# Kernel optimization log

Hardware: AMD Instinct MI355X
Metric: run time of the kernel (lower is better)

## Reference

```python
import jax, jax.numpy as jnp
import numpy as np

N = 100000   # num_rows
M = 50000    # num_cols
D = 32       # embed_dim
E = 5000000  # num observed edges


def setup_inputs() -> dict:
    key = jax.random.key(0)
    ks = jax.random.split(key, 9)
    bound = 1.0 / np.sqrt(D)
    row_embed = jax.random.uniform(ks[0], (N, D), minval=-bound, maxval=bound, dtype=jnp.float32)
    col_embed = jax.random.uniform(ks[1], (M, D), minval=-bound, maxval=bound, dtype=jnp.float32)
    # kaiming_uniform_ with nonlinearity='relu': bound = sqrt(6 / fan_in)
    kb = np.sqrt(6.0 / D)
    W0 = jax.random.uniform(ks[2], (D, D), minval=-kb, maxval=kb, dtype=jnp.float32)
    W1 = jax.random.uniform(ks[3], (D, D), minval=-kb, maxval=kb, dtype=jnp.float32)
    W2 = jax.random.uniform(ks[4], (D, D), minval=-kb, maxval=kb, dtype=jnp.float32)
    b0 = jnp.zeros((D,), jnp.float32)
    b1 = jnp.zeros((D,), jnp.float32)
    b2 = jnp.zeros((D,), jnp.float32)
    edge_index = jax.random.randint(ks[5], (2, E), 0, N + M, dtype=jnp.int64)
    return {"row_embed": row_embed, "col_embed": col_embed,
            "W0": W0, "b0": b0, "W1": W1, "b1": b1, "W2": W2, "b2": b2,
            "edge_index": edge_index}


def reference(row_embed, col_embed, W0, b0, W1, b1, W2, b2, edge_index):
    num_nodes = N + M
    x = jnp.concatenate([row_embed, col_embed], axis=0)  # [N+M, D]
    # add self loops
    loop = jnp.arange(num_nodes, dtype=edge_index.dtype)
    src = jnp.concatenate([edge_index[0], loop])
    dst = jnp.concatenate([edge_index[1], loop])
    for W, b in ((W0, b0), (W1, b1), (W2, b2)):
        h = x @ W.T + b                       # dense linear [N+M, D]
        msg = h[src]                          # gather source features [E+N+M, D]
        agg = jax.ops.segment_sum(msg, dst, num_segments=num_nodes)
        x = jax.nn.relu(agg)
    return (x[:N], x[N:])
```

## Files before the change

### kernel.cpp

```cpp
#include <hip/hip_runtime.h>
#include <hip/hip_fp16.h>

#define N_ROWS 100000
#define NNODES 150000
#define D 32
#define NEDGE 5000000
#define BINSHIFT 7
#define BINSZ 128
#define NBINS 1172
#define NBLK 512
#define SCT 1024
#define CPB ((NEDGE + NBLK - 1) / NBLK)
#define NCOUNTS (NBINS * NBLK)
#define SCAN_ITEMS 1024
#define NSCAN (NCOUNTS / SCAN_ITEMS)

#define NB 8
#define BDIV 18750

#define LIN_T 128
#define LIN_RPB 256
#define LIN_GRID ((NNODES + LIN_RPB - 1) / LIN_RPB)


__global__ void count_kernel(const int* __restrict__ dst, int* __restrict__ counts) {
    __shared__ int h[4 * NBINS];
    const int t = threadIdx.x;
    const int sub = ((t >> 6) & 3) * NBINS;
    for (int b = t; b < 4 * NBINS; b += SCT) h[b] = 0;
    __syncthreads();
    const int e0 = blockIdx.x * CPB;
    const int e1 = min(e0 + CPB, NEDGE);
    for (int i = e0 + t; i < e1; i += SCT) atomicAdd(&h[sub + (dst[i] >> BINSHIFT)], 1);
    __syncthreads();
    for (int b = t; b < NBINS; b += SCT)
        counts[b * NBLK + blockIdx.x] = h[b] + h[NBINS + b] + h[2 * NBINS + b] + h[3 * NBINS + b];
}


__global__ void scanA(const int* __restrict__ counts, int* __restrict__ partials) {
    __shared__ int s[256];
    const int t = threadIdx.x;
    const int base = blockIdx.x * SCAN_ITEMS + t * 4;
    int sum = 0;
#pragma unroll
    for (int k = 0; k < 4; ++k) sum += counts[base + k];
    s[t] = sum;
    __syncthreads();
    for (int off = 128; off > 0; off >>= 1) {
        if (t < off) s[t] += s[t + off];
        __syncthreads();
    }
    if (t == 0) partials[blockIdx.x] = s[0];
}

__global__ void scanB(int* __restrict__ partials) {
    __shared__ int s[256];
    __shared__ int carry;
    const int t = threadIdx.x;
    if (t == 0) carry = 0;
    __syncthreads();
    for (int c = 0; c < (NSCAN + 255) / 256; ++c) {
        int idx = c * 256 + t;
        int v = (idx < NSCAN) ? partials[idx] : 0;
        s[t] = v;
        __syncthreads();
        for (int off = 1; off < 256; off <<= 1) {
            int tmp = (t >= off) ? s[t - off] : 0;
            __syncthreads();
            s[t] += tmp;
            __syncthreads();
        }
        if (idx < NSCAN) partials[idx] = carry + s[t] - v;
        __syncthreads();
        if (t == 0) carry += s[255];
        __syncthreads();
    }
}

__global__ void scanC(const int* __restrict__ counts, const int* __restrict__ partials,
                      int* __restrict__ bases, int* __restrict__ binPtr) {
    __shared__ int s[256];
    const int t = threadIdx.x;
    const int base = blockIdx.x * SCAN_ITEMS + t * 4;
    int c[4];
    int sum = 0;
#pragma unroll
    for (int k = 0; k < 4; ++k) { c[k] = counts[base + k]; sum += c[k]; }
    s[t] = sum;
    __syncthreads();
    for (int off = 1; off < 256; off <<= 1) {
        int v = (t >= off) ? s[t - off] : 0;
        __syncthreads();
        s[t] += v;
        __syncthreads();
    }
    int run = partials[blockIdx.x] + ((t == 0) ? 0 : s[t - 1]);
#pragma unroll
    for (int k = 0; k < 4; ++k) {
        int idx = base + k;
        bases[idx] = run;
        if ((idx & (NBLK - 1)) == 0) binPtr[idx / NBLK] = run;
        run += c[k];
    }
    if (blockIdx.x == 0 && t == 0) binPtr[NBINS] = NEDGE;
}


__global__ void __launch_bounds__(SCT, 2)
scatter3(const int* __restrict__ src, const int* __restrict__ dst,
         const int* __restrict__ bases, unsigned int* __restrict__ binned) {
    __shared__ int cnt[NBINS];
    __shared__ int lb[NBINS + 1];
    __shared__ int gb[NBINS];
    __shared__ int ssum[SCT];
    __shared__ unsigned int staged[CPB];

    const int t = threadIdx.x;
    const int e0 = blockIdx.x * CPB;
    const int e1 = min(e0 + CPB, NEDGE);
    const int n = e1 - e0;

    for (int b = t; b < NBINS; b += SCT) {
        cnt[b] = 0;
        gb[b] = bases[b * NBLK + blockIdx.x];
    }
    __syncthreads();
    for (int i = e0 + t; i < e1; i += SCT) atomicAdd(&cnt[dst[i] >> BINSHIFT], 1);
    __syncthreads();

    const int i0 = 2 * t, i1 = 2 * t + 1;
    const int c0 = (i0 < NBINS) ? cnt[i0] : 0;
    const int c1 = (i1 < NBINS) ? cnt[i1] : 0;
    ssum[t] = c0 + c1;
    __syncthreads();
    for (int off = 1; off < SCT; off <<= 1) {
        int v = (t >= off) ? ssum[t - off] : 0;
        __syncthreads();
        ssum[t] += v;
        __syncthreads();
    }
    const int excl = (t == 0) ? 0 : ssum[t - 1];
    if (i0 < NBINS) lb[i0] = excl;
    if (i1 < NBINS) lb[i1] = excl + c0;
    if (t == 0) lb[NBINS] = n;
    __syncthreads();

    for (int b = t; b < NBINS; b += SCT) cnt[b] = lb[b];
    __syncthreads();
    for (int i = e0 + t; i < e1; i += SCT) {
        const int dv = dst[i];
        const int bn = dv >> BINSHIFT;
        const int slot = atomicAdd(&cnt[bn], 1);
        staged[slot] = ((unsigned)(dv & (BINSZ - 1)) << 18) | (unsigned)src[i];
    }
    __syncthreads();

    const int grp = t >> 4;
    const int lane = t & 15;
    for (int b = grp; b < NBINS; b += 64) {
        const int lo = lb[b];
        const int hi = lb[b + 1];
        const int gbase = gb[b] - lo;
        for (int s2 = lo + lane; s2 < hi; s2 += 16)
            binned[gbase + s2] = staged[s2];
    }
}


__global__ void fine_sort8(const int* __restrict__ binPtr, const unsigned int* __restrict__ binned,
                           int* __restrict__ qrowptr, int* __restrict__ srcSorted) {
    __shared__ int cnt[BINSZ * NB];
    __shared__ int cur[BINSZ * NB];
    const int t = threadIdx.x;
    const int bin = blockIdx.x;
    const int e0 = binPtr[bin];
    const int e1 = binPtr[bin + 1];

    cnt[t] = 0;
    __syncthreads();
    for (int e = e0 + t; e < e1; e += 1024) {
        const unsigned u = binned[e];
        const unsigned s = u & 0x3FFFFu;
        const int key = (int)((u >> 18) * NB) + (int)(s / BDIV);
        atomicAdd(&cnt[key], 1);
    }
    __syncthreads();
    cur[t] = cnt[t];
    __syncthreads();
    for (int off = 1; off < BINSZ * NB; off <<= 1) {
        int v = (t >= off) ? cur[t - off] : 0;
        __syncthreads();
        cur[t] += v;
        __syncthreads();
    }
    {
        const int excl = cur[t] - cnt[t];
        qrowptr[bin * (BINSZ * NB) + t] = e0 + excl;
        cur[t] = excl;
    }
    __syncthreads();
    for (int e = e0 + t; e < e1; e += 1024) {
        const unsigned u = binned[e];
        const unsigned s = u & 0x3FFFFu;
        const int key = (int)((u >> 18) * NB) + (int)(s / BDIV);
        const int p = atomicAdd(&cur[key], 1);
        srcSorted[e0 + p] = (int)s;
    }
    if (bin == 0 && t == 0) qrowptr[NBINS * (BINSZ * NB)] = NEDGE;
}


template <int MODE>
__global__ void __launch_bounds__(LIN_T)
linear_rows(const float* __restrict__ xa, const float* __restrict__ xb,
            const float* __restrict__ W, const float* __restrict__ b,
            __half* __restrict__ H) {
    __shared__ float xs[LIN_RPB * 33];
    __shared__ float Ws[32 * 36];
    __shared__ float bs[32];
    const int t = threadIdx.x;

    for (int i = t; i < 1024; i += LIN_T) {
        const int c = i >> 5, k = i & 31;
        Ws[k * 36 + c] = W[i];
    }
    if (t < 32) bs[t] = b[t];

    const long long ebase = (long long)blockIdx.x * (LIN_RPB * 32);
#pragma unroll 4
    for (int i = 0; i < (LIN_RPB * 32) / LIN_T; ++i) {
        const long long e = ebase + i * LIN_T + t;
        const int flat = i * LIN_T + t;
        float v = 0.0f;
        if (e < (long long)NNODES * 32) {
            if (MODE == 0) {
                v = (e < (long long)N_ROWS * 32) ? xa[e] : xb[e - (long long)N_ROWS * 32];
            } else {
                v = fmaxf(xa[e], 0.0f);
            }
        }
        xs[(flat >> 5) * 33 + (flat & 31)] = v;
    }
    __syncthreads();

    float a0[32], a1[32];
#pragma unroll
    for (int c = 0; c < 32; ++c) { a0[c] = bs[c]; a1[c] = bs[c]; }
    const int r0 = 2 * t, r1 = 2 * t + 1;
#pragma unroll
    for (int k = 0; k < 32; ++k) {
        const float x0 = xs[r0 * 33 + k];
        const float x1 = xs[r1 * 33 + k];
        const float4* wr = (const float4*)&Ws[k * 36];
#pragma unroll
        for (int q = 0; q < 8; ++q) {
            const float4 w = wr[q];
            a0[4 * q + 0] = fmaf(x0, w.x, a0[4 * q + 0]);
            a0[4 * q + 1] = fmaf(x0, w.y, a0[4 * q + 1]);
            a0[4 * q + 2] = fmaf(x0, w.z, a0[4 * q + 2]);
            a0[4 * q + 3] = fmaf(x0, w.w, a0[4 * q + 3]);
            a1[4 * q + 0] = fmaf(x1, w.x, a1[4 * q + 0]);
            a1[4 * q + 1] = fmaf(x1, w.y, a1[4 * q + 1]);
            a1[4 * q + 2] = fmaf(x1, w.z, a1[4 * q + 2]);
            a1[4 * q + 3] = fmaf(x1, w.w, a1[4 * q + 3]);
        }
    }
    __syncthreads();

    unsigned* os = (unsigned*)xs;
#pragma unroll
    for (int p = 0; p < 16; ++p) {
        __half2 h0 = __floats2half2_rn(a0[2 * p], a0[2 * p + 1]);
        __half2 h1 = __floats2half2_rn(a1[2 * p], a1[2 * p + 1]);
        os[r0 * 17 + p] = *(unsigned*)&h0;
        os[r1 * 17 + p] = *(unsigned*)&h1;
    }
    __syncthreads();
    unsigned* H2 = (unsigned*)H;
    const long long obase = (long long)blockIdx.x * (LIN_RPB * 16);
#pragma unroll 4
    for (int i = 0; i < (LIN_RPB * 16) / LIN_T; ++i) {
        const long long o = obase + i * LIN_T + t;
        const int flat = i * LIN_T + t;
        if (o < (long long)NNODES * 16)
            H2[o] = os[(flat >> 4) * 17 + (flat & 15)];
    }
}


template <bool RELU>
__global__ void agg_csr(const int* __restrict__ qrowptr, const int* __restrict__ srcSorted,
                        const __half* __restrict__ H, float* __restrict__ OUT) {
    const int tid = threadIdx.x;
    const int d = blockIdx.x * 16 + (tid >> 4);
    const int j = tid & 15;
    const unsigned int* __restrict__ H2 = (const unsigned int*)H;

    int e = qrowptr[d * NB];
    const int eEnd = qrowptr[d * NB + NB];
    float2 acc = __half22float2(((const __half2*)H)[d * 16 + j]);
    for (; e + 7 < eEnd; e += 8) {
        int s[8];
#pragma unroll
        for (int k = 0; k < 8; ++k) s[k] = srcSorted[e + k];
        unsigned int v[8];
#pragma unroll
        for (int k = 0; k < 8; ++k) v[k] = H2[s[k] * 16 + j];
#pragma unroll
        for (int k = 0; k < 8; ++k) {
            const float2 f = __half22float2(*(const __half2*)&v[k]);
            acc.x += f.x;
            acc.y += f.y;
        }
    }
    for (; e < eEnd; ++e) {
        const unsigned int v = H2[srcSorted[e] * 16 + j];
        const float2 f = __half22float2(*(const __half2*)&v);
        acc.x += f.x;
        acc.y += f.y;
    }
    if (RELU) { acc.x = fmaxf(acc.x, 0.0f); acc.y = fmaxf(acc.y, 0.0f); }
    ((float2*)OUT)[d * 16 + j] = acc;
}


extern "C" void kernel_launch(void* const* d_in, const int* in_sizes, int n_in,
                              void* d_out, int out_size, void* d_ws, size_t ws_size,
                              hipStream_t stream) {
    const float* row_embed = (const float*)d_in[0];
    const float* col_embed = (const float*)d_in[1];
    const float* W0 = (const float*)d_in[2];
    const float* b0 = (const float*)d_in[3];
    const float* W1 = (const float*)d_in[4];
    const float* b1 = (const float*)d_in[5];
    const float* W2 = (const float*)d_in[6];
    const float* b2 = (const float*)d_in[7];
    const int* ei = (const int*)d_in[8];
    const int* src = ei;
    const int* dst = ei + NEDGE;
    float* out = (float*)d_out;

    __half* H = (__half*)d_ws;
    float* B0 = (float*)(H + (size_t)NNODES * D);
    unsigned int* binned = (unsigned int*)(B0 + (size_t)NNODES * D);
    int* srcSorted = (int*)(binned + NEDGE);
    int* counts = srcSorted + NEDGE;
    int* bases = counts + NCOUNTS;
    int* partials = bases + NCOUNTS;
    int* binPtr = partials + NSCAN;
    int* qrowptr = counts;

    const int agg_grid = NNODES / 16;

    count_kernel<<<NBLK, SCT, 0, stream>>>(dst, counts);
    scanA<<<NSCAN, 256, 0, stream>>>(counts, partials);
    scanB<<<1, 256, 0, stream>>>(partials);
    scanC<<<NSCAN, 256, 0, stream>>>(counts, partials, bases, binPtr);
    scatter3<<<NBLK, SCT, 0, stream>>>(src, dst, bases, binned);
    fine_sort8<<<NBINS, 1024, 0, stream>>>(binPtr, binned, qrowptr, srcSorted);

    linear_rows<0><<<LIN_GRID, LIN_T, 0, stream>>>(row_embed, col_embed, W0, b0, H);
    agg_csr<false><<<agg_grid, 256, 0, stream>>>(qrowptr, srcSorted, H, B0);
    linear_rows<1><<<LIN_GRID, LIN_T, 0, stream>>>(B0, nullptr, W1, b1, H);
    agg_csr<false><<<agg_grid, 256, 0, stream>>>(qrowptr, srcSorted, H, B0);
    linear_rows<1><<<LIN_GRID, LIN_T, 0, stream>>>(B0, nullptr, W2, b2, H);
    agg_csr<true><<<agg_grid, 256, 0, stream>>>(qrowptr, srcSorted, H, out);

    (void)in_sizes; (void)n_in; (void)out_size; (void)ws_size;
}
```

Measured before the change: 376.4 us.

## Fuse next-layer linear into aggregation kernel and ping-pong half buffers

Folds the ReLU and the dense 32x32 linear of the next layer into the epilogue of the CSR aggregation kernel. Each block stages its 16 aggregated rows and the transposed weights in shared memory, then writes fp16 features straight into a second buffer. This removes two linear_rows launches and the fp32 intermediate round trip through global memory. Edge index loads are also made nontemporal. In exchange, each aggregation block carries extra shared memory, a weight load and a barrier.

```diff
diff --git a/kernel.cpp b/kernel.cpp
--- a/kernel.cpp
+++ b/kernel.cpp
@@ -288,22 +288,36 @@
     }
 }
 
-
-template <bool RELU>
-__global__ void agg_csr(const int* __restrict__ qrowptr, const int* __restrict__ srcSorted,
-                        const __half* __restrict__ H, float* __restrict__ OUT) {
+template <int MODE>
+__global__ void agg_fused2(const int* __restrict__ qrowptr, const int* __restrict__ srcSorted,
+                           const __half* __restrict__ Hin, const float* __restrict__ W,
+                           const float* __restrict__ b, __half* __restrict__ Hout,
+                           float* __restrict__ out) {
+    __shared__ float xs[16 * 33];
+    __shared__ float Ws[32 * 36];
+    __shared__ float bs[32];
     const int tid = threadIdx.x;
-    const int d = blockIdx.x * 16 + (tid >> 4);
+    const int r = tid >> 4;
     const int j = tid & 15;
-    const unsigned int* __restrict__ H2 = (const unsigned int*)H;
+
+    if (MODE == 0) {
+        for (int i = tid; i < 1024; i += 256) {
+            const int c = i >> 5, k = i & 31;
+            Ws[k * 36 + c] = W[i];
+        }
+        if (tid < 32) bs[tid] = b[tid];
+    }
+
+    const int d = blockIdx.x * 16 + r;
+    const unsigned int* __restrict__ H2 = (const unsigned int*)Hin;
 
     int e = qrowptr[d * NB];
     const int eEnd = qrowptr[d * NB + NB];
-    float2 acc = __half22float2(((const __half2*)H)[d * 16 + j]);
+    float2 acc = __half22float2(((const __half2*)Hin)[d * 16 + j]);
     for (; e + 7 < eEnd; e += 8) {
         int s[8];
 #pragma unroll
-        for (int k = 0; k < 8; ++k) s[k] = srcSorted[e + k];
+        for (int k = 0; k < 8; ++k) s[k] = __builtin_nontemporal_load(srcSorted + e + k);
         unsigned int v[8];
 #pragma unroll
         for (int k = 0; k < 8; ++k) v[k] = H2[s[k] * 16 + j];
@@ -315,13 +329,32 @@
         }
     }
     for (; e < eEnd; ++e) {
-        const unsigned int v = H2[srcSorted[e] * 16 + j];
+        const unsigned int v = H2[__builtin_nontemporal_load(srcSorted + e) * 16 + j];
         const float2 f = __half22float2(*(const __half2*)&v);
         acc.x += f.x;
         acc.y += f.y;
     }
-    if (RELU) { acc.x = fmaxf(acc.x, 0.0f); acc.y = fmaxf(acc.y, 0.0f); }
-    ((float2*)OUT)[d * 16 + j] = acc;
+
+    if (MODE == 1) {
+        acc.x = fmaxf(acc.x, 0.0f);
+        acc.y = fmaxf(acc.y, 0.0f);
+        ((float2*)out)[d * 16 + j] = acc;
+        return;
+    }
+
+    xs[r * 33 + 2 * j] = fmaxf(acc.x, 0.0f);
+    xs[r * 33 + 2 * j + 1] = fmaxf(acc.y, 0.0f);
+    __syncthreads();
+
+    float n0 = bs[2 * j], n1 = bs[2 * j + 1];
+#pragma unroll
+    for (int k = 0; k < 32; ++k) {
+        const float x = xs[r * 33 + k];
+        n0 = fmaf(x, Ws[k * 36 + 2 * j], n0);
+        n1 = fmaf(x, Ws[k * 36 + 2 * j + 1], n1);
+    }
+    __half2 h = __floats2half2_rn(n0, n1);
+    ((unsigned*)Hout)[d * 16 + j] = *(unsigned*)&h;
 }
 
 
@@ -341,9 +374,9 @@
     const int* dst = ei + NEDGE;
     float* out = (float*)d_out;
 
-    __half* H = (__half*)d_ws;
-    float* B0 = (float*)(H + (size_t)NNODES * D);
-    unsigned int* binned = (unsigned int*)(B0 + (size_t)NNODES * D);
+    __half* H0 = (__half*)d_ws;
+    __half* H1 = H0 + (size_t)NNODES * D;
+    unsigned int* binned = (unsigned int*)(H1 + (size_t)NNODES * D);
     int* srcSorted = (int*)(binned + NEDGE);
     int* counts = srcSorted + NEDGE;
     int* bases = counts + NCOUNTS;
@@ -360,12 +393,10 @@
     scatter3<<<NBLK, SCT, 0, stream>>>(src, dst, bases, binned);
     fine_sort8<<<NBINS, 1024, 0, stream>>>(binPtr, binned, qrowptr, srcSorted);
 
-    linear_rows<0><<<LIN_GRID, LIN_T, 0, stream>>>(row_embed, col_embed, W0, b0, H);
-    agg_csr<false><<<agg_grid, 256, 0, stream>>>(qrowptr, srcSorted, H, B0);
-    linear_rows<1><<<LIN_GRID, LIN_T, 0, stream>>>(B0, nullptr, W1, b1, H);
-    agg_csr<false><<<agg_grid, 256, 0, stream>>>(qrowptr, srcSorted, H, B0);
-    linear_rows<1><<<LIN_GRID, LIN_T, 0, stream>>>(B0, nullptr, W2, b2, H);
-    agg_csr<true><<<agg_grid, 256, 0, stream>>>(qrowptr, srcSorted, H, out);
+    linear_rows<0><<<LIN_GRID, LIN_T, 0, stream>>>(row_embed, col_embed, W0, b0, H0);
+    agg_fused2<0><<<agg_grid, 256, 0, stream>>>(qrowptr, srcSorted, H0, W1, b1, H1, nullptr);
+    agg_fused2<0><<<agg_grid, 256, 0, stream>>>(qrowptr, srcSorted, H1, W2, b2, H0, nullptr);
+    agg_fused2<1><<<agg_grid, 256, 0, stream>>>(qrowptr, srcSorted, H0, nullptr, nullptr, nullptr, out);
 
     (void)in_sizes; (void)n_in; (void)out_size; (void)ws_size;
 }
```

After: 376.8 us. Within noise of the previous version (+0.1%).
